# Optimization experiments

Measured on AMD Instinct MI355X. Metric: run time of the kernel, lower is better.

Reference implementation:

```python
import jax, jax.numpy as jnp
import numpy as np

NUM_ITERATIONS = 3
EPS = 1e-12


def _squash(s):
    # s: (..., V). squash(s) = |s|^2 * s / ((1+|s|^2) * |s|)
    sq = jnp.sum(s * s, axis=-1, keepdims=True)
    return sq * s / ((1.0 + sq) * jnp.sqrt(sq))


def setup_inputs() -> dict:
    key = jax.random.key(0)
    kx, kw = jax.random.split(key)
    B, L, P, V, Q = 16, 64, 1024, 64, 16
    x = jax.random.normal(kx, (B, P, Q), dtype=jnp.float32)
    W = 0.01 * jax.random.normal(kw, (L, P, V, Q), dtype=jnp.float32)
    return {"x": x, "W": W}


def reference(x, W):
    # u_hat[b,l,p,v] = sum_q W[l,p,v,q] * x[b,p,q]
    u_hat = jnp.einsum('lpvq,bpq->blpv', W, x)  # (B, L, P, V)
    B, L, P, V = u_hat.shape
    b_ij = jnp.zeros((B, L, P), dtype=u_hat.dtype)
    c_ij = None
    v = None
    for it in range(NUM_ITERATIONS):  # small fixed unroll
        c_ij = jax.nn.softmax(b_ij, axis=1)  # softmax over latent caps
        s = jnp.einsum('blp,blpv->blv', c_ij, u_hat)
        v = _squash(s)  # (B, L, V)
        if it < NUM_ITERATIONS - 1:
            # agreement update: b_ij += <v_j, u_hat>
            b_ij = b_ij + jnp.einsum('blv,blpv->blp', v, u_hat)
    # T-score: coupling entropy over latent axis, per primary capsule
    cT = jnp.swapaxes(c_ij, 1, 2)  # (B, P, L)
    entropy = -jnp.sum(cT * jnp.log(cT + EPS), axis=-1)  # (B, P)
    T = jnp.mean(1.0 - entropy / np.log(float(L)))
    # D-score: max over caps of population std (over batch) of activation norms
    v_norm = jnp.linalg.norm(v, axis=-1)  # (B, L)
    D = jnp.max(jnp.std(v_norm, axis=0))
    return v, T, D
```

## Files before the change

### kernel.cpp

```cpp
#include <hip/hip_runtime.h>
#include <hip/hip_bf16.h>

#define B 16
#define L 64
#define P 1024
#define V 64
#define Q 16
#define LN64 4.158883083359672f

#define CHBC 16
#define NCH_BC (P / CHBC)

typedef unsigned short ushort8_t __attribute__((ext_vector_type(8)));

static __device__ __forceinline__ float bf2f(ushort u) {
    return __uint_as_float(((unsigned int)u) << 16);
}
static __device__ __forceinline__ ushort f2bf(float f) {
    unsigned int x = __float_as_uint(f);
    unsigned int r = (x + 0x7fffu + ((x >> 16) & 1u)) >> 16;
    return (ushort)r;
}

static __device__ __forceinline__ float wsum64(float v) {
#pragma unroll
    for (int m = 32; m > 0; m >>= 1) v += __shfl_xor(v, m, 64);
    return v;
}
static __device__ __forceinline__ float wmax64(float v) {
#pragma unroll
    for (int m = 32; m > 0; m >>= 1) v = fmaxf(v, __shfl_xor(v, m, 64));
    return v;
}

__global__ __launch_bounds__(256) void k_uhat(const float* __restrict__ Wt,
                                              const float* __restrict__ x,
                                              ushort* __restrict__ uhat) {
    const int t = threadIdx.x;
    const int w = t >> 6;
    const int lane = t & 63;
    const int p = blockIdx.x >> 1;
    const int l0 = (blockIdx.x & 1) * 32;

    __shared__ float xs[B * Q];
    {
        const int b = t >> 4, q = t & 15;
        xs[t] = x[((size_t)b * P + p) * Q + q];
    }
    __syncthreads();

    float xr[4][Q];
#pragma unroll
    for (int i = 0; i < 4; ++i)
#pragma unroll
        for (int q = 0; q < Q; ++q) xr[i][q] = xs[(w * 4 + i) * Q + q];

    const float4* Wp0 = reinterpret_cast<const float4*>(Wt);

    float4 Wb[4][4];
#define LOADW(l, d)                                                          \
    {                                                                        \
        const float4* wp = Wp0 + (((size_t)(l) * P + p) * V + lane) * 4;     \
        d[0] = wp[0]; d[1] = wp[1]; d[2] = wp[2]; d[3] = wp[3];              \
    }
#define COMPUTE(l, Wr)                                                       \
    {                                                                        \
        _Pragma("unroll")                                                    \
        for (int i = 0; i < 4; ++i) {                                        \
            float u = 0.f;                                                   \
            _Pragma("unroll")                                                \
            for (int q4 = 0; q4 < 4; ++q4) {                                 \
                u = fmaf(Wr[q4].x, xr[i][q4 * 4 + 0], u);                    \
                u = fmaf(Wr[q4].y, xr[i][q4 * 4 + 1], u);                    \
                u = fmaf(Wr[q4].z, xr[i][q4 * 4 + 2], u);                    \
                u = fmaf(Wr[q4].w, xr[i][q4 * 4 + 3], u);                    \
            }                                                                \
            const int b = w * 4 + i;                                         \
            uhat[(((size_t)(b * L + (l))) * P + p) * V + lane] = f2bf(u);    \
        }                                                                    \
    }

    LOADW(l0 + 0, Wb[0]);
    LOADW(l0 + 1, Wb[1]);
    LOADW(l0 + 2, Wb[2]);
    LOADW(l0 + 3, Wb[3]);
#pragma unroll
    for (int li = 0; li < 32; ++li) {
        COMPUTE(l0 + li, Wb[li & 3]);
        if (li + 4 < 32) LOADW(l0 + li + 4, Wb[li & 3]);
    }
#undef LOADW
#undef COMPUTE
}

__global__ __launch_bounds__(256) void k_s(const ushort* __restrict__ uhat,
                                           float* __restrict__ vout) {
    const int l = blockIdx.x, b = blockIdx.y;
    const int t = threadIdx.x;
    const int w = t >> 6, lane = t & 63;
    const int pl = t >> 4;
    const int vg = t & 15;

    __shared__ float4 sl[4][16];

    const ushort* up = uhat + ((size_t)(b * L + l)) * P * V + (size_t)pl * V + vg * 4;

    float4 acc = {0.f, 0.f, 0.f, 0.f};
#pragma unroll 8
    for (int i = 0; i < 64; ++i) {
        ushort4 u = *reinterpret_cast<const ushort4*>(up + (size_t)i * 16 * V);
        acc.x += bf2f(u.x); acc.y += bf2f(u.y);
        acc.z += bf2f(u.z); acc.w += bf2f(u.w);
    }
    acc.x *= (1.f / 64.f); acc.y *= (1.f / 64.f);
    acc.z *= (1.f / 64.f); acc.w *= (1.f / 64.f);
#pragma unroll
    for (int m = 16; m <= 32; m <<= 1) {
        acc.x += __shfl_xor(acc.x, m, 64);
        acc.y += __shfl_xor(acc.y, m, 64);
        acc.z += __shfl_xor(acc.z, m, 64);
        acc.w += __shfl_xor(acc.w, m, 64);
    }
    if (lane < 16) sl[w][vg] = acc;
    __syncthreads();
    if (w == 0 && lane < 16) {
        float4 s0 = sl[0][vg], s1 = sl[1][vg], s2 = sl[2][vg], s3 = sl[3][vg];
        float4 s;
        s.x = s0.x + s1.x + s2.x + s3.x;
        s.y = s0.y + s1.y + s2.y + s3.y;
        s.z = s0.z + s1.z + s2.z + s3.z;
        s.w = s0.w + s1.w + s2.w + s3.w;
        float sq = s.x * s.x + s.y * s.y + s.z * s.z + s.w * s.w;
        sq += __shfl_xor(sq, 1, 64);
        sq += __shfl_xor(sq, 2, 64);
        sq += __shfl_xor(sq, 4, 64);
        sq += __shfl_xor(sq, 8, 64);
        float f = sqrtf(sq) / (1.0f + sq);
        float4 o = {s.x * f, s.y * f, s.z * f, s.w * f};
        *reinterpret_cast<float4*>(vout + (size_t)(b * L + l) * V + vg * 4) = o;
    }
}

__global__ __launch_bounds__(512, 4) void k_bc(const ushort* __restrict__ uhat,
                                               const float* __restrict__ vv,
                                               float* __restrict__ bbuf,
                                               float* __restrict__ sp,
                                               float* __restrict__ Tsum,
                                               int add_prev, int do_T) {
    const int ch = blockIdx.x, b = blockIdx.y;
    const int p0 = ch * CHBC;
    const int t = threadIdx.x;
    const int w = t >> 6, lane = t & 63;
    const int pl8 = lane >> 3;
    const int vg8 = lane & 7;
    const int l0 = w * 8;

    __shared__ float vsh[L][V];
    __shared__ float bl[CHBC][L + 1];
    __shared__ float twv[8];

    {
        const float4* vvp = reinterpret_cast<const float4*>(vv + (size_t)b * L * V);
        float4* vshp = reinterpret_cast<float4*>(&vsh[0][0]);
#pragma unroll
        for (int i = 0; i < 2; ++i) vshp[t + i * 512] = vvp[t + i * 512];
    }

    ushort8_t ur[8][2];
    {
        const ushort* ubase = uhat + (((size_t)(b * L + l0)) * P + p0 + pl8) * V + vg8 * 8;
#pragma unroll
        for (int li = 0; li < 8; ++li) {
#pragma unroll
            for (int ph = 0; ph < 2; ++ph)
                ur[li][ph] = *reinterpret_cast<const ushort8_t*>(
                    ubase + ((size_t)li * P + ph * 8) * V);
        }
    }
    __syncthreads();

#pragma unroll
    for (int li = 0; li < 8; ++li) {
        const int l = l0 + li;
        const float4 va = *reinterpret_cast<const float4*>(&vsh[l][vg8 * 8]);
        const float4 vb = *reinterpret_cast<const float4*>(&vsh[l][vg8 * 8 + 4]);
#pragma unroll
        for (int ph = 0; ph < 2; ++ph) {
            float d;
            d = bf2f(ur[li][ph][0]) * va.x;
            d = fmaf(bf2f(ur[li][ph][1]), va.y, d);
            d = fmaf(bf2f(ur[li][ph][2]), va.z, d);
            d = fmaf(bf2f(ur[li][ph][3]), va.w, d);
            d = fmaf(bf2f(ur[li][ph][4]), vb.x, d);
            d = fmaf(bf2f(ur[li][ph][5]), vb.y, d);
            d = fmaf(bf2f(ur[li][ph][6]), vb.z, d);
            d = fmaf(bf2f(ur[li][ph][7]), vb.w, d);
            d += __shfl_xor(d, 1, 64);
            d += __shfl_xor(d, 2, 64);
            d += __shfl_xor(d, 4, 64);
            if (vg8 == 0) bl[ph * 8 + pl8][l] = d;
        }
    }
    __syncthreads();

    float tloc = 0.f;
#pragma unroll
    for (int pi = 0; pi < 2; ++pi) {
        const int pli = w * 2 + pi;
        const int p = p0 + pli;
        float bv = bl[pli][lane];
        float* bp = bbuf + ((size_t)b * P + p) * L;
        if (add_prev) bv += bp[lane];
        bp[lane] = bv;
        float m = wmax64(bv);
        float e = __expf(bv - m);
        float ssum = wsum64(e);
        float cc = e / ssum;
        bl[pli][lane] = cc;
        if (do_T) tloc += cc * __logf(64.0f * (cc + 1e-12f));
    }
    if (do_T) {
        float dsum = wsum64(tloc);
        if (lane == 0) twv[w] = dsum;
    }
    __syncthreads();
    if (do_T && t == 0) {
        float s8 = twv[0] + twv[1] + twv[2] + twv[3] +
                   twv[4] + twv[5] + twv[6] + twv[7];
        atomicAdd(Tsum, s8 * (1.0f / LN64));
    }

    float* spb = sp + (size_t)(b * NCH_BC + ch) * L * V;
#pragma unroll
    for (int li = 0; li < 8; ++li) {
        const int l = l0 + li;
        const float cA = bl[pl8][l];
        const float cB = bl[8 + pl8][l];
        float4 pa, pb;
        pa.x = cA * bf2f(ur[li][0][0]) + cB * bf2f(ur[li][1][0]);
        pa.y = cA * bf2f(ur[li][0][1]) + cB * bf2f(ur[li][1][1]);
        pa.z = cA * bf2f(ur[li][0][2]) + cB * bf2f(ur[li][1][2]);
        pa.w = cA * bf2f(ur[li][0][3]) + cB * bf2f(ur[li][1][3]);
        pb.x = cA * bf2f(ur[li][0][4]) + cB * bf2f(ur[li][1][4]);
        pb.y = cA * bf2f(ur[li][0][5]) + cB * bf2f(ur[li][1][5]);
        pb.z = cA * bf2f(ur[li][0][6]) + cB * bf2f(ur[li][1][6]);
        pb.w = cA * bf2f(ur[li][0][7]) + cB * bf2f(ur[li][1][7]);
#pragma unroll
        for (int m = 8; m <= 32; m <<= 1) {
            pa.x += __shfl_xor(pa.x, m, 64);
            pa.y += __shfl_xor(pa.y, m, 64);
            pa.z += __shfl_xor(pa.z, m, 64);
            pa.w += __shfl_xor(pa.w, m, 64);
            pb.x += __shfl_xor(pb.x, m, 64);
            pb.y += __shfl_xor(pb.y, m, 64);
            pb.z += __shfl_xor(pb.z, m, 64);
            pb.w += __shfl_xor(pb.w, m, 64);
        }
        if (pl8 == 0) {
            *reinterpret_cast<float4*>(spb + (size_t)l * V + vg8 * 8) = pa;
            *reinterpret_cast<float4*>(spb + (size_t)l * V + vg8 * 8 + 4) = pb;
        }
    }
}

__global__ __launch_bounds__(256) void k_v(const float* __restrict__ sp,
                                           float* __restrict__ vout,
                                           float* __restrict__ norms) {
    const int b = blockIdx.y;
    const int w = threadIdx.x >> 6, lane = threadIdx.x & 63;
    const int l = blockIdx.x * 4 + w;
    const float* p = sp + ((size_t)b * NCH_BC * L + l) * V + lane;
    float s = 0.f;
#pragma unroll 8
    for (int ch = 0; ch < NCH_BC; ++ch) s += p[(size_t)ch * L * V];
    float sq = wsum64(s * s);
    float f = sqrtf(sq) / (1.0f + sq);
    vout[((size_t)b * L + l) * V + lane] = s * f;
    if (norms && lane == 0) norms[b * L + l] = sq / (1.0f + sq);
}

__global__ void k_final(const float* __restrict__ Tsum,
                        const float* __restrict__ norms,
                        float* __restrict__ out) {
    const int lane = threadIdx.x & 63;
    float n[B];
    float sum = 0.f;
#pragma unroll
    for (int b = 0; b < B; ++b) { n[b] = norms[b * L + lane]; sum += n[b]; }
    const float mean = sum * (1.0f / B);
    float var = 0.f;
#pragma unroll
    for (int b = 0; b < B; ++b) { float d = n[b] - mean; var = fmaf(d, d, var); }
    var *= (1.0f / B);
    float sd = sqrtf(var);
    float D = wmax64(sd);
    if (lane == 0) {
        out[B * L * V] = Tsum[0] * (1.0f / (B * P));
        out[B * L * V + 1] = D;
    }
}

extern "C" void kernel_launch(void* const* d_in, const int* in_sizes, int n_in,
                              void* d_out, int out_size, void* d_ws, size_t ws_size,
                              hipStream_t stream) {
    const float* x = (const float*)d_in[0];
    const float* W = (const float*)d_in[1];
    float* out = (float*)d_out;

    char* ws = (char*)d_ws;
    ushort* uhat = (ushort*)ws;
    size_t off = (size_t)B * L * P * V * 2;
    float* spbuf = (float*)(ws + off); off += (size_t)B * NCH_BC * L * V * 4;
    float* vbuf  = (float*)(ws + off); off += (size_t)B * L * V * 4;
    float* bbuf  = (float*)(ws + off); off += (size_t)B * P * L * 4;
    float* norms = (float*)(ws + off); off += (size_t)B * L * 4;
    float* Tsum  = (float*)(ws + off); off += 256;

    hipMemsetAsync(Tsum, 0, sizeof(float), stream);

    hipLaunchKernelGGL(k_uhat, dim3(2048), dim3(256), 0, stream, W, x, uhat);
    hipLaunchKernelGGL(k_s, dim3(L, B), dim3(256), 0, stream, uhat, vbuf);
    hipLaunchKernelGGL(k_bc, dim3(NCH_BC, B), dim3(512), 0, stream,
                       uhat, vbuf, bbuf, spbuf, Tsum, 0, 0);
    hipLaunchKernelGGL(k_v, dim3(L / 4, B), dim3(256), 0, stream,
                       spbuf, vbuf, (float*)nullptr);
    hipLaunchKernelGGL(k_bc, dim3(NCH_BC, B), dim3(512), 0, stream,
                       uhat, vbuf, bbuf, spbuf, Tsum, 1, 1);
    hipLaunchKernelGGL(k_v, dim3(L / 4, B), dim3(256), 0, stream,
                       spbuf, out, norms);
    hipLaunchKernelGGL(k_final, dim3(1), dim3(64), 0, stream, Tsum, norms, out);
}
```

Before: 251.6 us.

## Stage W tiles through LDS with async global_load_lds triple buffering

In the u_hat kernel, the register-based four-deep prefetch of W is replaced by direct global-to-LDS loads (`__builtin_amdgcn_global_load_lds`) into a per-wave ring of three LDS slots. Each iteration waits with explicit `s_waitcnt vmcnt` counts, issues the load two latent capsules ahead, then reads the current tile from LDS and computes. The goal is to free the VGPRs that held prefetched W and keep more memory traffic in flight on this bandwidth-bound kernel. The cost is extra LDS reads per iteration. The hand-written vmcnt thresholds are fragile because the uhat stores may also be counted by vmcnt on this architecture, so a wait could pass before its tile has arrived.

Measured after the change: 259.4 us. +3.1%, slower.

```diff
diff --git a/kernel.cpp b/kernel.cpp
--- a/kernel.cpp
+++ b/kernel.cpp
@@ -12,6 +12,9 @@
 #define NCH_BC (P / CHBC)
 
 typedef unsigned short ushort8_t __attribute__((ext_vector_type(8)));
+
+typedef const __attribute__((address_space(1))) void* gld_gptr_t;
+typedef __attribute__((address_space(3))) void* gld_lptr_t;
 
 static __device__ __forceinline__ float bf2f(ushort u) {
     return __uint_as_float(((unsigned int)u) << 16);
@@ -43,7 +46,9 @@
     const int l0 = (blockIdx.x & 1) * 32;
 
     __shared__ float xs[B * Q];
-    {
+    __shared__ float4 wst[4][3][4][64];
+
+    if (t < B * Q) {
         const int b = t >> 4, q = t & 15;
         xs[t] = x[((size_t)b * P + p) * Q + q];
     }
@@ -55,41 +60,69 @@
 #pragma unroll
         for (int q = 0; q < Q; ++q) xr[i][q] = xs[(w * 4 + i) * Q + q];
 
-    const float4* Wp0 = reinterpret_cast<const float4*>(Wt);
-
-    float4 Wb[4][4];
-#define LOADW(l, d)                                                          \
-    {                                                                        \
-        const float4* wp = Wp0 + (((size_t)(l) * P + p) * V + lane) * 4;     \
-        d[0] = wp[0]; d[1] = wp[1]; d[2] = wp[2]; d[3] = wp[3];              \
-    }
-#define COMPUTE(l, Wr)                                                       \
-    {                                                                        \
-        _Pragma("unroll")                                                    \
-        for (int i = 0; i < 4; ++i) {                                        \
-            float u = 0.f;                                                   \
-            _Pragma("unroll")                                                \
-            for (int q4 = 0; q4 < 4; ++q4) {                                 \
-                u = fmaf(Wr[q4].x, xr[i][q4 * 4 + 0], u);                    \
-                u = fmaf(Wr[q4].y, xr[i][q4 * 4 + 1], u);                    \
-                u = fmaf(Wr[q4].z, xr[i][q4 * 4 + 2], u);                    \
-                u = fmaf(Wr[q4].w, xr[i][q4 * 4 + 3], u);                    \
-            }                                                                \
-            const int b = w * 4 + i;                                         \
-            uhat[(((size_t)(b * L + (l))) * P + p) * V + lane] = f2bf(u);    \
-        }                                                                    \
-    }
-
-    LOADW(l0 + 0, Wb[0]);
-    LOADW(l0 + 1, Wb[1]);
-    LOADW(l0 + 2, Wb[2]);
-    LOADW(l0 + 3, Wb[3]);
-#pragma unroll
-    for (int li = 0; li < 32; ++li) {
-        COMPUTE(l0 + li, Wb[li & 3]);
-        if (li + 4 < 32) LOADW(l0 + li + 4, Wb[li & 3]);
-    }
-#undef LOADW
+    const char* gbase = (const char*)(Wt + ((size_t)l0 * P + p) * (V * Q)) + lane * 64;
+    const size_t LSTRIDE = (size_t)P * V * Q * 4;
+    char* ldsb = (char*)&wst[w][0][0][0];
+
+#define STAGE(li, slot)                                                       \
+    {                                                                         \
+        const char* g = gbase + (size_t)(li) * LSTRIDE;                       \
+        char* lb = ldsb + (slot) * 4096;                                      \
+        __builtin_amdgcn_global_load_lds((gld_gptr_t)(g + 0),  (gld_lptr_t)(lb + 0),    16, 0, 0); \
+        __builtin_amdgcn_global_load_lds((gld_gptr_t)(g + 16), (gld_lptr_t)(lb + 1024), 16, 0, 0); \
+        __builtin_amdgcn_global_load_lds((gld_gptr_t)(g + 32), (gld_lptr_t)(lb + 2048), 16, 0, 0); \
+        __builtin_amdgcn_global_load_lds((gld_gptr_t)(g + 48), (gld_lptr_t)(lb + 3072), 16, 0, 0); \
+    }
+
+#define COMPUTE(li, slot)                                                     \
+    {                                                                         \
+        const float4* wr = (const float4*)(ldsb + (slot) * 4096);             \
+        const float4 W0 = wr[0 * 64 + lane];                                  \
+        const float4 W1 = wr[1 * 64 + lane];                                  \
+        const float4 W2 = wr[2 * 64 + lane];                                  \
+        const float4 W3 = wr[3 * 64 + lane];                                  \
+        _Pragma("unroll")                                                     \
+        for (int i = 0; i < 4; ++i) {                                         \
+            float u = 0.f;                                                    \
+            u = fmaf(W0.x, xr[i][0],  u); u = fmaf(W0.y, xr[i][1],  u);       \
+            u = fmaf(W0.z, xr[i][2],  u); u = fmaf(W0.w, xr[i][3],  u);       \
+            u = fmaf(W1.x, xr[i][4],  u); u = fmaf(W1.y, xr[i][5],  u);       \
+            u = fmaf(W1.z, xr[i][6],  u); u = fmaf(W1.w, xr[i][7],  u);       \
+            u = fmaf(W2.x, xr[i][8],  u); u = fmaf(W2.y, xr[i][9],  u);       \
+            u = fmaf(W2.z, xr[i][10], u); u = fmaf(W2.w, xr[i][11], u);       \
+            u = fmaf(W3.x, xr[i][12], u); u = fmaf(W3.y, xr[i][13], u);       \
+            u = fmaf(W3.z, xr[i][14], u); u = fmaf(W3.w, xr[i][15], u);       \
+            const int b = w * 4 + i;                                          \
+            uhat[(((size_t)(b * L + (l0 + (li)))) * P + p) * V + lane] = f2bf(u); \
+        }                                                                     \
+    }
+
+    STAGE(0, 0);
+    STAGE(1, 1);
+
+    asm volatile("s_waitcnt vmcnt(4)" ::: "memory");
+    __builtin_amdgcn_sched_barrier(0);
+    STAGE(2, 2);
+    COMPUTE(0, 0);
+
+    asm volatile("s_waitcnt vmcnt(8)" ::: "memory");
+    __builtin_amdgcn_sched_barrier(0);
+    STAGE(3, 0);
+    COMPUTE(1, 1);
+
+#pragma unroll 3
+    for (int li = 2; li <= 30; ++li) {
+        asm volatile("s_waitcnt vmcnt(12)" ::: "memory");
+        __builtin_amdgcn_sched_barrier(0);
+        if (li <= 29) STAGE(li + 2, (li + 2) % 3);
+        COMPUTE(li, li % 3);
+    }
+
+    asm volatile("s_waitcnt vmcnt(8)" ::: "memory");
+    __builtin_amdgcn_sched_barrier(0);
+    COMPUTE(31, 31 % 3);
+
+#undef STAGE
 #undef COMPUTE
 }
 
```

## Stream W through LDS with async global_load_lds pipeline in u_hat kernel

Applied to the files above, without the earlier changes.

Rewrites the u_hat kernel so W tiles are copied asynchronously from global memory straight into a six-slot LDS ring buffer using global_load_lds, with vmcnt waits and barriers forming a multi-stage pipeline. It also changes the thread mapping so each thread produces 8 consecutive v outputs for one batch row, packed into a single 16-byte bf16 store, and uses an XOR swizzle to avoid LDS bank conflicts. The intent is to overlap W loads with compute, shrink the register footprint, and widen the uhat stores. The trade-off is an extra barrier per stage and reliance on hand-written waitcnt counts.

Result: faster. 230.1 us (-8.6%).

```diff
diff --git a/kernel.cpp b/kernel.cpp
--- a/kernel.cpp
+++ b/kernel.cpp
@@ -12,6 +12,9 @@
 #define NCH_BC (P / CHBC)
 
 typedef unsigned short ushort8_t __attribute__((ext_vector_type(8)));
+
+typedef const __attribute__((address_space(1))) void* gld_gptr_t;
+typedef __attribute__((address_space(3))) void* gld_lptr_t;
 
 static __device__ __forceinline__ float bf2f(ushort u) {
     return __uint_as_float(((unsigned int)u) << 16);
@@ -41,56 +44,94 @@
     const int lane = t & 63;
     const int p = blockIdx.x >> 1;
     const int l0 = (blockIdx.x & 1) * 32;
+    const int b   = (t >> 3) & 15;
+    const int vo  = t & 7;
+    const int lih = t >> 7;
+    const int vosw = vo & 3;
 
     __shared__ float xs[B * Q];
+    __shared__ char wls[6][4096];
+
     {
-        const int b = t >> 4, q = t & 15;
-        xs[t] = x[((size_t)b * P + p) * Q + q];
-    }
-    __syncthreads();
-
-    float xr[4][Q];
-#pragma unroll
-    for (int i = 0; i < 4; ++i)
-#pragma unroll
-        for (int q = 0; q < Q; ++q) xr[i][q] = xs[(w * 4 + i) * Q + q];
-
-    const float4* Wp0 = reinterpret_cast<const float4*>(Wt);
-
-    float4 Wb[4][4];
-#define LOADW(l, d)                                                          \
-    {                                                                        \
-        const float4* wp = Wp0 + (((size_t)(l) * P + p) * V + lane) * 4;     \
-        d[0] = wp[0]; d[1] = wp[1]; d[2] = wp[2]; d[3] = wp[3];              \
-    }
-#define COMPUTE(l, Wr)                                                       \
-    {                                                                        \
-        _Pragma("unroll")                                                    \
-        for (int i = 0; i < 4; ++i) {                                        \
-            float u = 0.f;                                                   \
-            _Pragma("unroll")                                                \
-            for (int q4 = 0; q4 < 4; ++q4) {                                 \
-                u = fmaf(Wr[q4].x, xr[i][q4 * 4 + 0], u);                    \
-                u = fmaf(Wr[q4].y, xr[i][q4 * 4 + 1], u);                    \
-                u = fmaf(Wr[q4].z, xr[i][q4 * 4 + 2], u);                    \
-                u = fmaf(Wr[q4].w, xr[i][q4 * 4 + 3], u);                    \
-            }                                                                \
-            const int b = w * 4 + i;                                         \
-            uhat[(((size_t)(b * L + (l))) * P + p) * V + lane] = f2bf(u);    \
-        }                                                                    \
-    }
-
-    LOADW(l0 + 0, Wb[0]);
-    LOADW(l0 + 1, Wb[1]);
-    LOADW(l0 + 2, Wb[2]);
-    LOADW(l0 + 3, Wb[3]);
-#pragma unroll
-    for (int li = 0; li < 32; ++li) {
-        COMPUTE(l0 + li, Wb[li & 3]);
-        if (li + 4 < 32) LOADW(l0 + li + 4, Wb[li & 3]);
-    }
-#undef LOADW
+        const int bb = t >> 4, q = t & 15;
+        xs[t] = x[((size_t)bb * P + p) * Q + q];
+    }
+    __syncthreads();
+
+    float xr[16];
+    {
+        const float4* xb = reinterpret_cast<const float4*>(&xs[b * Q]);
+#pragma unroll
+        for (int q4 = 0; q4 < 4; ++q4) {
+            float4 v4 = xb[q4];
+            xr[q4 * 4 + 0] = v4.x; xr[q4 * 4 + 1] = v4.y;
+            xr[q4 * 4 + 2] = v4.z; xr[q4 * 4 + 3] = v4.w;
+        }
+    }
+
+    const int sc = w * 64 + lane;
+    const int nsrc = (sc & ~3) | ((sc & 3) ^ ((sc >> 5) & 3));
+    const char* gW = (const char*)Wt + ((size_t)l0 * P + p) * (V * Q * 4)
+                     + (size_t)nsrc * 16;
+    const size_t LSTRIDE = (size_t)P * V * Q * 4;
+
+    ushort* ub = uhat + ((size_t)(b * L + l0) * P + p) * V + vo * 8;
+
+#define STAGE(li_)                                                            \
+    __builtin_amdgcn_global_load_lds(                                         \
+        (gld_gptr_t)(gW + (size_t)(li_) * LSTRIDE),                           \
+        (gld_lptr_t)(&wls[(li_) % 6][w * 1024]), 16, 0, 0);
+
+#define COMPUTE(s)                                                            \
+    {                                                                         \
+        const char* sb = &wls[(2 * (s)) % 6][0] + lih * 4096;                 \
+        float d[8];                                                           \
+        _Pragma("unroll")                                                     \
+        for (int j = 0; j < 8; ++j) {                                         \
+            const char* rb = sb + (vo * 8 + j) * 64;                          \
+            const float4 W0 = *(const float4*)(rb + ((0 ^ vosw) << 4));       \
+            const float4 W1 = *(const float4*)(rb + ((1 ^ vosw) << 4));       \
+            const float4 W2 = *(const float4*)(rb + ((2 ^ vosw) << 4));       \
+            const float4 W3 = *(const float4*)(rb + ((3 ^ vosw) << 4));       \
+            float u = 0.f;                                                    \
+            u = fmaf(W0.x, xr[0],  u); u = fmaf(W0.y, xr[1],  u);             \
+            u = fmaf(W0.z, xr[2],  u); u = fmaf(W0.w, xr[3],  u);             \
+            u = fmaf(W1.x, xr[4],  u); u = fmaf(W1.y, xr[5],  u);             \
+            u = fmaf(W1.z, xr[6],  u); u = fmaf(W1.w, xr[7],  u);             \
+            u = fmaf(W2.x, xr[8],  u); u = fmaf(W2.y, xr[9],  u);             \
+            u = fmaf(W2.z, xr[10], u); u = fmaf(W2.w, xr[11], u);             \
+            u = fmaf(W3.x, xr[12], u); u = fmaf(W3.y, xr[13], u);             \
+            u = fmaf(W3.z, xr[14], u); u = fmaf(W3.w, xr[15], u);             \
+            d[j] = u;                                                         \
+        }                                                                     \
+        uint4 pk;                                                             \
+        pk.x = (unsigned)f2bf(d[0]) | ((unsigned)f2bf(d[1]) << 16);           \
+        pk.y = (unsigned)f2bf(d[2]) | ((unsigned)f2bf(d[3]) << 16);           \
+        pk.z = (unsigned)f2bf(d[4]) | ((unsigned)f2bf(d[5]) << 16);           \
+        pk.w = (unsigned)f2bf(d[6]) | ((unsigned)f2bf(d[7]) << 16);           \
+        *reinterpret_cast<uint4*>(ub + (size_t)(2 * (s) + lih) * P * V) = pk; \
+    }
+
+#define WAITB(N)                                                              \
+    asm volatile("s_waitcnt vmcnt(" #N ")" ::: "memory");                     \
+    __builtin_amdgcn_sched_barrier(0);                                        \
+    __builtin_amdgcn_s_barrier();                                             \
+    __builtin_amdgcn_sched_barrier(0);
+
+    STAGE(0); STAGE(1); STAGE(2); STAGE(3);
+
+    WAITB(2); STAGE(4); STAGE(5); COMPUTE(0);
+    WAITB(3); STAGE(6); STAGE(7); COMPUTE(1);
+#pragma unroll
+    for (int s = 2; s <= 13; ++s) {
+        WAITB(4); STAGE(2 * s + 4); STAGE(2 * s + 5); COMPUTE(s);
+    }
+    WAITB(4); COMPUTE(14);
+    WAITB(2); COMPUTE(15);
+
+#undef STAGE
 #undef COMPUTE
+#undef WAITB
 }
 
 __global__ __launch_bounds__(256) void k_s(const ushort* __restrict__ uhat,
```

## Compute u_hat with bf16 MFMA, async LDS staging, and fused first-iteration sums

Applied to the files above, without the earlier changes.

Rewrites the u_hat kernel to use 16x16x32 bf16 MFMA instructions. Weight tiles are staged through a triple-buffered LDS ring using global_load_lds with explicit vmcnt waits, and x is converted to bf16 fragments. Each u_hat slice is recovered as the difference between successive accumulator values, and the running accumulators are written as per-chunk partial sums for the first routing iteration. This removes the separate k_s pass that reread all of u_hat. The trade-off is a bf16-rounded x and W plus accumulation-difference rounding, and a larger partial-sum buffer that k_v must now reduce over 128 chunks.

After: 241.7 us. 3.9% less time.

```diff
diff --git a/kernel.cpp b/kernel.cpp
--- a/kernel.cpp
+++ b/kernel.cpp
@@ -10,8 +10,14 @@
 
 #define CHBC 16
 #define NCH_BC (P / CHBC)
+#define LPV ((size_t)L * P * V)
 
 typedef unsigned short ushort8_t __attribute__((ext_vector_type(8)));
+typedef __attribute__((ext_vector_type(8))) short bf16x8;
+typedef __attribute__((ext_vector_type(4))) float f32x4;
+
+typedef const __attribute__((address_space(1))) void* gld_gptr_t;
+typedef __attribute__((address_space(3))) void* gld_lptr_t;
 
 static __device__ __forceinline__ float bf2f(ushort u) {
     return __uint_as_float(((unsigned int)u) << 16);
@@ -21,6 +27,9 @@
     unsigned int r = (x + 0x7fffu + ((x >> 16) & 1u)) >> 16;
     return (ushort)r;
 }
+static __device__ __forceinline__ unsigned pk2(float lo, float hi) {
+    return (unsigned)f2bf(lo) | ((unsigned)f2bf(hi) << 16);
+}
 
 static __device__ __forceinline__ float wsum64(float v) {
 #pragma unroll
@@ -33,112 +42,163 @@
     return v;
 }
 
-__global__ __launch_bounds__(256) void k_uhat(const float* __restrict__ Wt,
-                                              const float* __restrict__ x,
-                                              ushort* __restrict__ uhat) {
+union FragU { uint4 u; bf16x8 s; };
+
+__global__ __launch_bounds__(256, 3) void k_uhat(const float* __restrict__ Wt,
+                                                 const float* __restrict__ x,
+                                                 ushort* __restrict__ uhat,
+                                                 float* __restrict__ sp0) {
     const int t = threadIdx.x;
     const int w = t >> 6;
     const int lane = t & 63;
-    const int p = blockIdx.x >> 1;
-    const int l0 = (blockIdx.x & 1) * 32;
-
-    __shared__ float xs[B * Q];
+    const int kb = lane >> 4;
+    const int cc = lane & 15;
+    const int ch = blockIdx.x;
+    const int l = blockIdx.y;
+    const int p0 = ch * 32;
+
+    __shared__ __align__(16) char smem[49152];
+    unsigned int* xstage = (unsigned int*)smem;
+
+#pragma unroll
+    for (int i = 0; i < 16; ++i) {
+        const int e = i * 256 + t;
+        const int pp = e >> 7, ln = (e >> 2) & 31, m = e & 3;
+        const int b = ln & 15, qb = (ln >> 4) * 8;
+        const float2 xv = *reinterpret_cast<const float2*>(
+            x + ((size_t)b * P + p0 + pp) * Q + qb + 2 * m);
+        xstage[e] = pk2(xv.x, xv.y);
+    }
+    __syncthreads();
+
+    uint4 af[8];
+#pragma unroll
+    for (int i = 0; i < 8; ++i) {
+        if (lane < 32)
+            af[i] = *reinterpret_cast<const uint4*>(
+                smem + ((size_t)(w * 8 + i) * 32 + lane) * 16);
+        else
+            af[i] = (uint4){0u, 0u, 0u, 0u};
+    }
+    __syncthreads();
+
+    char* ring = smem + w * 12288;
+    const int sperm = (lane & ~3) | ((lane & 3) ^ ((lane >> 3) & 3));
+    const char* gW = (const char*)(Wt + ((size_t)l * P + p0 + w * 8) * (V * Q))
+                     + (size_t)sperm * 16;
+    const int xk = (cc >> 1) & 3;
+
+    f32x4 cacc0 = {0.f, 0.f, 0.f, 0.f}, cacc1 = {0.f, 0.f, 0.f, 0.f};
+    f32x4 cacc2 = {0.f, 0.f, 0.f, 0.f}, cacc3 = {0.f, 0.f, 0.f, 0.f};
+
+#define STAGE(i_)                                                             \
+    {                                                                         \
+        const char* s_ = gW + (size_t)(i_) * 4096;                            \
+        char* d_ = ring + ((i_) % 3) * 4096;                                  \
+        __builtin_amdgcn_global_load_lds((gld_gptr_t)(s_ + 0),                \
+                                         (gld_lptr_t)(d_ + 0), 16, 0, 0);     \
+        __builtin_amdgcn_global_load_lds((gld_gptr_t)(s_ + 1024),             \
+                                         (gld_lptr_t)(d_ + 1024), 16, 0, 0);  \
+        __builtin_amdgcn_global_load_lds((gld_gptr_t)(s_ + 2048),             \
+                                         (gld_lptr_t)(d_ + 2048), 16, 0, 0);  \
+        __builtin_amdgcn_global_load_lds((gld_gptr_t)(s_ + 3072),             \
+                                         (gld_lptr_t)(d_ + 3072), 16, 0, 0);  \
+    }
+
+#define BFRAG(g_, dst_)                                                       \
+    {                                                                         \
+        if (lane < 32) {                                                      \
+            const char* rb_ = ring + (slot_) * 4096 + (cc + 16 * (g_)) * 64;  \
+            const float4 f0 =                                                 \
+                *(const float4*)(rb_ + (((2 * kb + 0) ^ xk) << 4));           \
+            const float4 f1 =                                                 \
+                *(const float4*)(rb_ + (((2 * kb + 1) ^ xk) << 4));           \
+            dst_.u = (uint4){pk2(f0.x, f0.y), pk2(f0.z, f0.w),                \
+                             pk2(f1.x, f1.y), pk2(f1.z, f1.w)};               \
+        } else {                                                              \
+            dst_.u = (uint4){0u, 0u, 0u, 0u};                                 \
+        }                                                                     \
+    }
+
+#define MMGROUP(g_, cacc_)                                                    \
+    {                                                                         \
+        FragU bf_;                                                            \
+        BFRAG(g_, bf_);                                                       \
+        f32x4 d_ = __builtin_amdgcn_mfma_f32_16x16x32_bf16(afr.s, bf_.s,      \
+                                                           cacc_, 0, 0, 0);   \
+        f32x4 u_ = d_ - cacc_;                                                \
+        cacc_ = d_;                                                           \
+        const unsigned lo01_ = pk2(u_[0], u_[1]);                             \
+        const unsigned lo23_ = pk2(u_[2], u_[3]);                             \
+        ushort* up_ = ub_ + (g_) * 16;                                        \
+        up_[0] = (ushort)lo01_;                                               \
+        up_[LPV] = (ushort)(lo01_ >> 16);                                     \
+        up_[2 * LPV] = (ushort)lo23_;                                         \
+        up_[3 * LPV] = (ushort)(lo23_ >> 16);                                 \
+    }
+
+#define COMPUTE(i_)                                                           \
+    {                                                                         \
+        const int slot_ = (i_) % 3;                                           \
+        const int p_ = p0 + w * 8 + (i_);                                     \
+        FragU afr; afr.u = af[i_];                                            \
+        ushort* ub_ = uhat +                                                  \
+            (((size_t)(kb * 4) * L + l) * P + p_) * V + cc;                   \
+        MMGROUP(0, cacc0);                                                    \
+        MMGROUP(1, cacc1);                                                    \
+        MMGROUP(2, cacc2);                                                    \
+        MMGROUP(3, cacc3);                                                    \
+    }
+
+#define WAITV(N)                                                              \
+    asm volatile("s_waitcnt vmcnt(" #N ")" ::: "memory");                     \
+    __builtin_amdgcn_sched_barrier(0);
+
+    STAGE(0); STAGE(1);
+    WAITV(4);  STAGE(2); COMPUTE(0);
+    WAITV(16); STAGE(3); COMPUTE(1);
+    WAITV(32); STAGE(4); COMPUTE(2);
+    WAITV(32); STAGE(5); COMPUTE(3);
+    WAITV(32); STAGE(6); COMPUTE(4);
+    WAITV(32); STAGE(7); COMPUTE(5);
+    WAITV(32); COMPUTE(6);
+    WAITV(28); COMPUTE(7);
+
     {
-        const int b = t >> 4, q = t & 15;
-        xs[t] = x[((size_t)b * P + p) * Q + q];
-    }
-    __syncthreads();
-
-    float xr[4][Q];
-#pragma unroll
-    for (int i = 0; i < 4; ++i)
-#pragma unroll
-        for (int q = 0; q < Q; ++q) xr[i][q] = xs[(w * 4 + i) * Q + q];
-
-    const float4* Wp0 = reinterpret_cast<const float4*>(Wt);
-
-    float4 Wb[4][4];
-#define LOADW(l, d)                                                          \
-    {                                                                        \
-        const float4* wp = Wp0 + (((size_t)(l) * P + p) * V + lane) * 4;     \
-        d[0] = wp[0]; d[1] = wp[1]; d[2] = wp[2]; d[3] = wp[3];              \
-    }
-#define COMPUTE(l, Wr)                                                       \
-    {                                                                        \
-        _Pragma("unroll")                                                    \
-        for (int i = 0; i < 4; ++i) {                                        \
-            float u = 0.f;                                                   \
-            _Pragma("unroll")                                                \
-            for (int q4 = 0; q4 < 4; ++q4) {                                 \
-                u = fmaf(Wr[q4].x, xr[i][q4 * 4 + 0], u);                    \
-                u = fmaf(Wr[q4].y, xr[i][q4 * 4 + 1], u);                    \
-                u = fmaf(Wr[q4].z, xr[i][q4 * 4 + 2], u);                    \
-                u = fmaf(Wr[q4].w, xr[i][q4 * 4 + 3], u);                    \
-            }                                                                \
-            const int b = w * 4 + i;                                         \
-            uhat[(((size_t)(b * L + (l))) * P + p) * V + lane] = f2bf(u);    \
-        }                                                                    \
-    }
-
-    LOADW(l0 + 0, Wb[0]);
-    LOADW(l0 + 1, Wb[1]);
-    LOADW(l0 + 2, Wb[2]);
-    LOADW(l0 + 3, Wb[3]);
-#pragma unroll
-    for (int li = 0; li < 32; ++li) {
-        COMPUTE(l0 + li, Wb[li & 3]);
-        if (li + 4 < 32) LOADW(l0 + li + 4, Wb[li & 3]);
-    }
-#undef LOADW
+        float* sb = sp0 + (((size_t)l * 128 + ch * 4 + w) * 16) * 64;
+#pragma unroll
+        for (int i2 = 0; i2 < 4; ++i2) {
+            const int b = kb * 4 + i2;
+            sb[(size_t)b * 64 + cc + 0]  = cacc0[i2];
+            sb[(size_t)b * 64 + cc + 16] = cacc1[i2];
+            sb[(size_t)b * 64 + cc + 32] = cacc2[i2];
+            sb[(size_t)b * 64 + cc + 48] = cacc3[i2];
+        }
+    }
+#undef STAGE
+#undef BFRAG
+#undef MMGROUP
 #undef COMPUTE
-}
-
-__global__ __launch_bounds__(256) void k_s(const ushort* __restrict__ uhat,
-                                           float* __restrict__ vout) {
-    const int l = blockIdx.x, b = blockIdx.y;
-    const int t = threadIdx.x;
-    const int w = t >> 6, lane = t & 63;
-    const int pl = t >> 4;
-    const int vg = t & 15;
-
-    __shared__ float4 sl[4][16];
-
-    const ushort* up = uhat + ((size_t)(b * L + l)) * P * V + (size_t)pl * V + vg * 4;
-
-    float4 acc = {0.f, 0.f, 0.f, 0.f};
+#undef WAITV
+}
+
+__global__ __launch_bounds__(256) void k_v(const float* __restrict__ sp,
+                                           size_t cb, size_t cl, size_t cs,
+                                           int nch, float scale,
+                                           float* __restrict__ vout,
+                                           float* __restrict__ norms) {
+    const int b = blockIdx.y;
+    const int w = threadIdx.x >> 6, lane = threadIdx.x & 63;
+    const int l = blockIdx.x * 4 + w;
+    const float* p = sp + cb * b + cl * l + lane;
+    float s = 0.f;
 #pragma unroll 8
-    for (int i = 0; i < 64; ++i) {
-        ushort4 u = *reinterpret_cast<const ushort4*>(up + (size_t)i * 16 * V);
-        acc.x += bf2f(u.x); acc.y += bf2f(u.y);
-        acc.z += bf2f(u.z); acc.w += bf2f(u.w);
-    }
-    acc.x *= (1.f / 64.f); acc.y *= (1.f / 64.f);
-    acc.z *= (1.f / 64.f); acc.w *= (1.f / 64.f);
-#pragma unroll
-    for (int m = 16; m <= 32; m <<= 1) {
-        acc.x += __shfl_xor(acc.x, m, 64);
-        acc.y += __shfl_xor(acc.y, m, 64);
-        acc.z += __shfl_xor(acc.z, m, 64);
-        acc.w += __shfl_xor(acc.w, m, 64);
-    }
-    if (lane < 16) sl[w][vg] = acc;
-    __syncthreads();
-    if (w == 0 && lane < 16) {
-        float4 s0 = sl[0][vg], s1 = sl[1][vg], s2 = sl[2][vg], s3 = sl[3][vg];
-        float4 s;
-        s.x = s0.x + s1.x + s2.x + s3.x;
-        s.y = s0.y + s1.y + s2.y + s3.y;
-        s.z = s0.z + s1.z + s2.z + s3.z;
-        s.w = s0.w + s1.w + s2.w + s3.w;
-        float sq = s.x * s.x + s.y * s.y + s.z * s.z + s.w * s.w;
-        sq += __shfl_xor(sq, 1, 64);
-        sq += __shfl_xor(sq, 2, 64);
-        sq += __shfl_xor(sq, 4, 64);
-        sq += __shfl_xor(sq, 8, 64);
-        float f = sqrtf(sq) / (1.0f + sq);
-        float4 o = {s.x * f, s.y * f, s.z * f, s.w * f};
-        *reinterpret_cast<float4*>(vout + (size_t)(b * L + l) * V + vg * 4) = o;
-    }
+    for (int ch = 0; ch < nch; ++ch) s += p[(size_t)ch * cs];
+    s *= scale;
+    float sq = wsum64(s * s);
+    float f = sqrtf(sq) / (1.0f + sq);
+    vout[((size_t)b * L + l) * V + lane] = s * f;
+    if (norms && lane == 0) norms[b * L + l] = sq / (1.0f + sq);
 }
 
 __global__ __launch_bounds__(512, 4) void k_bc(const ushort* __restrict__ uhat,
@@ -263,22 +323,6 @@
     }
 }
 
-__global__ __launch_bounds__(256) void k_v(const float* __restrict__ sp,
-                                           float* __restrict__ vout,
-                                           float* __restrict__ norms) {
-    const int b = blockIdx.y;
-    const int w = threadIdx.x >> 6, lane = threadIdx.x & 63;
-    const int l = blockIdx.x * 4 + w;
-    const float* p = sp + ((size_t)b * NCH_BC * L + l) * V + lane;
-    float s = 0.f;
-#pragma unroll 8
-    for (int ch = 0; ch < NCH_BC; ++ch) s += p[(size_t)ch * L * V];
-    float sq = wsum64(s * s);
-    float f = sqrtf(sq) / (1.0f + sq);
-    vout[((size_t)b * L + l) * V + lane] = s * f;
-    if (norms && lane == 0) norms[b * L + l] = sq / (1.0f + sq);
-}
-
 __global__ void k_final(const float* __restrict__ Tsum,
                         const float* __restrict__ norms,
                         float* __restrict__ out) {
@@ -310,7 +354,8 @@
     char* ws = (char*)d_ws;
     ushort* uhat = (ushort*)ws;
     size_t off = (size_t)B * L * P * V * 2;
-    float* spbuf = (float*)(ws + off); off += (size_t)B * NCH_BC * L * V * 4;
+    float* spbuf = (float*)(ws + off);
+    off += (size_t)64 * 128 * 16 * 64 * 4;
     float* vbuf  = (float*)(ws + off); off += (size_t)B * L * V * 4;
     float* bbuf  = (float*)(ws + off); off += (size_t)B * P * L * 4;
     float* norms = (float*)(ws + off); off += (size_t)B * L * 4;
@@ -318,15 +363,19 @@
 
     hipMemsetAsync(Tsum, 0, sizeof(float), stream);
 
-    hipLaunchKernelGGL(k_uhat, dim3(2048), dim3(256), 0, stream, W, x, uhat);
-    hipLaunchKernelGGL(k_s, dim3(L, B), dim3(256), 0, stream, uhat, vbuf);
+    hipLaunchKernelGGL(k_uhat, dim3(32, 64), dim3(256), 0, stream, W, x, uhat, spbuf);
+    hipLaunchKernelGGL(k_v, dim3(L / 4, B), dim3(256), 0, stream,
+                       spbuf, (size_t)64, (size_t)131072, (size_t)1024, 128,
+                       1.0f / 64.0f, vbuf, (float*)nullptr);
     hipLaunchKernelGGL(k_bc, dim3(NCH_BC, B), dim3(512), 0, stream,
                        uhat, vbuf, bbuf, spbuf, Tsum, 0, 0);
     hipLaunchKernelGGL(k_v, dim3(L / 4, B), dim3(256), 0, stream,
-                       spbuf, vbuf, (float*)nullptr);
+                       spbuf, (size_t)NCH_BC * L * V, (size_t)V, (size_t)L * V,
+                       NCH_BC, 1.0f, vbuf, (float*)nullptr);
     hipLaunchKernelGGL(k_bc, dim3(NCH_BC, B), dim3(512), 0, stream,
                        uhat, vbuf, bbuf, spbuf, Tsum, 1, 1);
     hipLaunchKernelGGL(k_v, dim3(L / 4, B), dim3(256), 0, stream,
-                       spbuf, out, norms);
+                       spbuf, (size_t)NCH_BC * L * V, (size_t)V, (size_t)L * V,
+                       NCH_BC, 1.0f, out, norms);
     hipLaunchKernelGGL(k_final, dim3(1), dim3(64), 0, stream, Tsum, norms, out);
 }
```
